# Kernel optimization log

Hardware: AMD Instinct MI355X
Metric: run time of the kernel (lower is better)

## Reference

```python
import jax, jax.numpy as jnp
import numpy as np

B, N, C, D = 64, 1024, 128, 64

def setup_inputs() -> dict:
    key = jax.random.key(0)
    ks = jax.random.split(key, 7)
    # kaiming_normal_ on weights (fan_in = C), default zero-ish biases kept as Linear default uniform; use small uniform
    std = float(np.sqrt(2.0 / C))
    bb = float(1.0 / np.sqrt(C))
    return {
        "x": jax.random.normal(ks[0], (B, N, C), jnp.float32),
        "Wq": jax.random.normal(ks[1], (C, D), jnp.float32) * std,
        "bq": jax.random.uniform(ks[2], (D,), jnp.float32, -bb, bb),
        "Wk": jax.random.normal(ks[3], (C, D), jnp.float32) * std,
        "bk": jax.random.uniform(ks[4], (D,), jnp.float32, -bb, bb),
        "Wv": jax.random.normal(ks[5], (C, D), jnp.float32) * std,
        "bv": jax.random.uniform(ks[6], (D,), jnp.float32, -bb, bb),
    }

def reference(x, Wq, bq, Wk, bk, Wv, bv):
    q = jax.nn.relu(jnp.einsum('bnc,cd->bnd', x, Wq) + bq)  # [B,N,D]
    k = jax.nn.relu(jnp.einsum('bnc,cd->bnd', x, Wk) + bk)
    v = jax.nn.relu(jnp.einsum('bnc,cd->bnd', x, Wv) + bv)
    scores = jnp.einsum('bnd,bmd->bnm', q, k) / jnp.sqrt(jnp.asarray(D, q.dtype))
    attn = jax.nn.softmax(scores, axis=-1)
    out = jnp.einsum('bnm,bmd->bnd', attn, v)
    return out + q
```

## Files before the change

kernel.cpp:

```cpp
#include <hip/hip_runtime.h>
#include <hip/hip_bf16.h>


#define Bsz 64
#define Nsz 1024
#define Csz 128
#define Dsz 64

typedef __attribute__((ext_vector_type(8))) short short8;
typedef __attribute__((ext_vector_type(4))) float f32x4;

__device__ __forceinline__ unsigned short f2bf(float f) {
    union { float f; unsigned u; } v; v.f = f;
    unsigned r = v.u + 0x7FFF + ((v.u >> 16) & 1);
    return (unsigned short)(r >> 16);
}
__device__ __forceinline__ float bf2f(unsigned short h) {
    union { unsigned u; float f; } v; v.u = ((unsigned)h) << 16;
    return v.f;
}
__device__ __forceinline__ unsigned pack_bf16rn(float lo, float hi) {
    unsigned ulo = __float_as_uint(lo) + 0x8000u;
    unsigned uhi = __float_as_uint(hi) + 0x8000u;
    return __builtin_amdgcn_perm(uhi, ulo, 0x07060302u);
}

#define SCq (0.125f * 1.44269504f)
#define INV_SC (1.0f / (0.125f * 1.44269504f))

__global__ __launch_bounds__(256) void wprep_kernel(
    const float* __restrict__ Wq, const float* __restrict__ Wk,
    const float* __restrict__ Wv, unsigned short* __restrict__ wfrag)
{
    int t = blockIdx.x * 256 + threadIdx.x;
    int lane = t & 63, ksi = (t >> 6) & 3, dt = t >> 8;
    int l16 = lane & 15, quad = lane >> 4;
    int d = dt * 16 + l16;
    int c0 = ksi * 32 + quad * 8;
    short8 h8, l8, k8, v8;
    #pragma unroll
    for (int j = 0; j < 8; j++) {
        float w = Wq[(c0 + j) * Dsz + d];
        unsigned short h = f2bf(w);
        h8[j] = (short)h;
        l8[j] = (short)f2bf(w - bf2f(h));
        k8[j] = (short)f2bf(Wk[(c0 + j) * Dsz + d]);
        v8[j] = (short)f2bf(Wv[(c0 + j) * Dsz + d]);
    }
    int idx = (dt * 4 + ksi) * 64 + lane;
    ((short8*)wfrag)[0 * 1024 + idx] = h8;
    ((short8*)wfrag)[1 * 1024 + idx] = l8;
    ((short8*)wfrag)[2 * 1024 + idx] = k8;
    ((short8*)wfrag)[3 * 1024 + idx] = v8;
}

__global__ __launch_bounds__(256) void qkv_kernel(
    const float* __restrict__ x, const unsigned short* __restrict__ wfrag,
    const float* __restrict__ bq, const float* __restrict__ bk,
    const float* __restrict__ bv,
    unsigned short* __restrict__ qs, unsigned short* __restrict__ ks2,
    unsigned short* __restrict__ vt2)
{
    __shared__ short xh[8192];
    __shared__ short xl[8192];
    const int t    = threadIdx.x;
    const int lane = t & 63;
    const int l16  = lane & 15, quad = lane >> 4;
    const int dt   = t >> 6;
    const int blk = blockIdx.x;
    const int r8  = blk & 7;
    const int m   = blk >> 3;
    const int bat = r8 + 8 * (m >> 4);
    const int til = m & 15;
    const long rowbase = ((long)bat * 16 + til) * 64;
    const int d = dt * 16 + l16;

    short8 wqh[4], wql[4], wkf[4], wvf[4];
    #pragma unroll
    for (int ksi = 0; ksi < 4; ksi++) {
        int idx = (dt * 4 + ksi) * 64 + lane;
        wqh[ksi] = ((const short8*)wfrag)[0 * 1024 + idx];
        wql[ksi] = ((const short8*)wfrag)[1 * 1024 + idx];
        wkf[ksi] = ((const short8*)wfrag)[2 * 1024 + idx];
        wvf[ksi] = ((const short8*)wfrag)[3 * 1024 + idx];
    }

    {
        const int row = t & 63;
        const float* xrow = x + (rowbase + row) * Csz;
        #pragma unroll
        for (int p = 0; p < 4; p++) {
            int cb = (t >> 6) + p * 4;
            float4 a = *(const float4*)(xrow + cb * 8);
            float4 bb = *(const float4*)(xrow + cb * 8 + 4);
            float f[8] = {a.x, a.y, a.z, a.w, bb.x, bb.y, bb.z, bb.w};
            short8 hi, lo;
            #pragma unroll
            for (int i = 0; i < 8; i++) {
                unsigned short h = f2bf(f[i]);
                hi[i] = (short)h;
                lo[i] = (short)f2bf(f[i] - bf2f(h));
            }
            int unit = ((row >> 4) * 4 + (cb >> 2)) * 64 + ((row & 15) | ((cb & 3) << 4));
            *(short8*)&xh[unit * 8] = hi;
            *(short8*)&xl[unit * 8] = lo;
        }
    }
    __syncthreads();

    f32x4 aq[4], ak[4], av[4];
    #pragma unroll
    for (int i = 0; i < 4; i++) {
        aq[i] = (f32x4){0.f, 0.f, 0.f, 0.f};
        ak[i] = (f32x4){0.f, 0.f, 0.f, 0.f};
        av[i] = (f32x4){0.f, 0.f, 0.f, 0.f};
    }
    #pragma unroll
    for (int ksi = 0; ksi < 4; ksi++) {
        #pragma unroll
        for (int rt = 0; rt < 4; rt++) {
            short8 ah = *(const short8*)&xh[((rt * 4 + ksi) * 64 + lane) * 8];
            short8 al = *(const short8*)&xl[((rt * 4 + ksi) * 64 + lane) * 8];
            aq[rt] = __builtin_amdgcn_mfma_f32_16x16x32_bf16(ah, wqh[ksi], aq[rt], 0, 0, 0);
            aq[rt] = __builtin_amdgcn_mfma_f32_16x16x32_bf16(al, wqh[ksi], aq[rt], 0, 0, 0);
            aq[rt] = __builtin_amdgcn_mfma_f32_16x16x32_bf16(ah, wql[ksi], aq[rt], 0, 0, 0);
            ak[rt] = __builtin_amdgcn_mfma_f32_16x16x32_bf16(ah, wkf[ksi], ak[rt], 0, 0, 0);
            av[rt] = __builtin_amdgcn_mfma_f32_16x16x32_bf16(ah, wvf[ksi], av[rt], 0, 0, 0);
        }
    }

    const float bqd = bq[d], bkd = bk[d], bvd = bv[d];
    const long b  = rowbase >> 10;
    const int  kt = (int)((rowbase >> 6) & 15);

    const int half  = dt >> 1;
    const int quadk = ((dt & 1) << 1) | (l16 >> 3);
    const int jk    = l16 & 7;
    unsigned short* kbase = ks2 + ((((long)(b * 16 + kt) * 4) * 2 + half) * 64) * 8;

    float vv[4][4];
    #pragma unroll
    for (int rt = 0; rt < 4; rt++) {
        #pragma unroll
        for (int r = 0; r < 4; r++) {
            long n = rowbase + rt * 16 + quad * 4 + r;
            float q = fmaxf(aq[rt][r] + bqd, 0.f);
            float k = fmaxf(ak[rt][r] + bkd, 0.f);
            vv[r][rt] = fmaxf(av[rt][r] + bvd, 0.f);
            qs[n * Dsz + d] = f2bf(q * SCq);
            kbase[((long)rt * 2 * 64 + quadk * 16 + quad * 4 + r) * 8 + jk] = f2bf(k);
        }
    }
    const int ck = quad >> 1;
    const int quadp = (quad & 1) * 2;
    long vidx = (((long)(b * 16 + kt) * 4 + dt) * 2 + ck) * 64 + quadp * 16 + l16;
    uint4 o0 = make_uint4(pack_bf16rn(vv[0][0], vv[0][1]), pack_bf16rn(vv[0][2], vv[0][3]),
                          pack_bf16rn(vv[1][0], vv[1][1]), pack_bf16rn(vv[1][2], vv[1][3]));
    uint4 o1 = make_uint4(pack_bf16rn(vv[2][0], vv[2][1]), pack_bf16rn(vv[2][2], vv[2][3]),
                          pack_bf16rn(vv[3][0], vv[3][1]), pack_bf16rn(vv[3][2], vv[3][3]));
    ((uint4*)vt2)[vidx]      = o0;
    ((uint4*)vt2)[vidx + 16] = o1;
}

__global__ __launch_bounds__(256) void attn_kernel(
    const unsigned short* __restrict__ qs,
    const unsigned short* __restrict__ ks2,
    const unsigned short* __restrict__ vt2,
    float* __restrict__ out)
{
    __shared__ short Pl[4][32][72];

    const int t    = threadIdx.x;
    const int wave = t >> 6;
    const int lane = t & 63;
    const int l16  = lane & 15;
    const int quad = lane >> 4;
    const int b    = blockIdx.x & 63;
    const int qh   = blockIdx.x >> 6;
    const int qbase = qh * 128 + wave * 32;

    const short8* ks8 = (const short8*)ks2 + (long)b * (16 * 4 * 2 * 64);
    const short8* vt8 = (const short8*)vt2 + (long)b * (16 * 4 * 2 * 64);

    short8 aq[2][2];
    #pragma unroll
    for (int s = 0; s < 2; s++) {
        const unsigned short* qp = qs + ((long)b * Nsz + qbase + s * 16 + l16) * Dsz + quad * 8;
        aq[s][0] = *(const short8*)(qp);
        aq[s][1] = *(const short8*)(qp + 32);
    }

    f32x4 O[2][4];
    float lsum[2][4];
    #pragma unroll
    for (int s = 0; s < 2; s++)
        #pragma unroll
        for (int i = 0; i < 4; i++) { O[s][i] = (f32x4){0.f,0.f,0.f,0.f}; lsum[s][i] = 0.f; }

    short8 kf[4][2];
    #pragma unroll
    for (int kb = 0; kb < 4; kb++) {
        kf[kb][0] = ks8[(kb * 2 + 0) * 64 + lane];
        kf[kb][1] = ks8[(kb * 2 + 1) * 64 + lane];
    }

    for (int kt = 0; kt < 16; kt++) {
        short8 bvf[2][4];
        #pragma unroll
        for (int cb = 0; cb < 4; cb++) {
            bvf[0][cb] = vt8[((long)kt * 8 + cb * 2 + 0) * 64 + lane];
            bvf[1][cb] = vt8[((long)kt * 8 + cb * 2 + 1) * 64 + lane];
        }

        f32x4 sc[2][4];
        #pragma unroll
        for (int s = 0; s < 2; s++) {
            #pragma unroll
            for (int kb = 0; kb < 4; kb++) {
                f32x4 z = (f32x4){0.f, 0.f, 0.f, 0.f};
                z = __builtin_amdgcn_mfma_f32_16x16x32_bf16(aq[s][0], kf[kb][0], z, 0, 0, 0);
                z = __builtin_amdgcn_mfma_f32_16x16x32_bf16(aq[s][1], kf[kb][1], z, 0, 0, 0);
                sc[s][kb] = z;
            }
        }

        short8 kf2[4][2];
        {
            int ktn = (kt + 1) & 15;
            #pragma unroll
            for (int kb = 0; kb < 4; kb++) {
                kf2[kb][0] = ks8[((long)ktn * 8 + kb * 2 + 0) * 64 + lane];
                kf2[kb][1] = ks8[((long)ktn * 8 + kb * 2 + 1) * 64 + lane];
            }
        }

        #pragma unroll
        for (int s = 0; s < 2; s++) {
            #pragma unroll
            for (int r = 0; r < 4; r++) {
                float p0 = __builtin_amdgcn_exp2f(sc[s][0][r]);
                float p1 = __builtin_amdgcn_exp2f(sc[s][1][r]);
                float p2 = __builtin_amdgcn_exp2f(sc[s][2][r]);
                float p3 = __builtin_amdgcn_exp2f(sc[s][3][r]);
                lsum[s][r] += (p0 + p1) + (p2 + p3);
                *(uint2*)&Pl[wave][s * 16 + quad * 4 + r][l16 * 4] =
                    make_uint2(pack_bf16rn(p0, p1), pack_bf16rn(p2, p3));
            }
        }

        #pragma unroll
        for (int ck = 0; ck < 2; ck++) {
            #pragma unroll
            for (int s = 0; s < 2; s++) {
                short8 ap = *(const short8*)&Pl[wave][s * 16 + l16][ck * 32 + quad * 8];
                #pragma unroll
                for (int cb = 0; cb < 4; cb++) {
                    O[s][cb] = __builtin_amdgcn_mfma_f32_16x16x32_bf16(ap, bvf[ck][cb], O[s][cb], 0, 0, 0);
                }
            }
        }

        #pragma unroll
        for (int kb = 0; kb < 4; kb++) { kf[kb][0] = kf2[kb][0]; kf[kb][1] = kf2[kb][1]; }
    }

    #pragma unroll
    for (int s = 0; s < 2; s++)
        #pragma unroll
        for (int r = 0; r < 4; r++)
            #pragma unroll
            for (int off = 1; off < 16; off <<= 1)
                lsum[s][r] += __shfl_xor(lsum[s][r], off);

    #pragma unroll
    for (int s = 0; s < 2; s++) {
        #pragma unroll
        for (int r = 0; r < 4; r++) {
            float rl = 1.0f / lsum[s][r];
            long nrow = (long)b * Nsz + qbase + s * 16 + quad * 4 + r;
            #pragma unroll
            for (int cb = 0; cb < 4; cb++) {
                int d = cb * 16 + l16;
                float qv = bf2f(qs[nrow * Dsz + d]) * INV_SC;
                out[nrow * Dsz + d] = O[s][cb][r] * rl + qv;
            }
        }
    }
}

extern "C" void kernel_launch(void* const* d_in, const int* in_sizes, int n_in,
                              void* d_out, int out_size, void* d_ws, size_t ws_size,
                              hipStream_t stream) {
    const float* x  = (const float*)d_in[0];
    const float* Wq = (const float*)d_in[1];
    const float* bq = (const float*)d_in[2];
    const float* Wk = (const float*)d_in[3];
    const float* bk = (const float*)d_in[4];
    const float* Wv = (const float*)d_in[5];
    const float* bv = (const float*)d_in[6];
    float* out = (float*)d_out;

    char* ws = (char*)d_ws;
    unsigned short* qsc   = (unsigned short*)ws;
    unsigned short* ks2   = (unsigned short*)(ws + 0x1000000);
    unsigned short* vt2   = (unsigned short*)(ws + 0x2000000);
    unsigned short* wfrag = (unsigned short*)(ws + 0x3000000);

    wprep_kernel<<<dim3(4), dim3(256), 0, stream>>>(Wq, Wk, Wv, wfrag);
    qkv_kernel<<<dim3(1024), dim3(256), 0, stream>>>(
        x, wfrag, bq, bk, bv, qsc, ks2, vt2);
    attn_kernel<<<dim3(512), dim3(256), 0, stream>>>(
        qsc, ks2, vt2, out);
}
```

Measured before the change: 122.8 us.

## Stage K/V tiles into LDS via async global_load_lds double buffering

The attention kernel now loads each K and V tile into a double-buffered LDS array with global_load_lds, split across waves: two waves fetch K and two fetch V. All four waves then read fragments from LDS instead of each wave loading them redundantly from global memory into registers. K is now stored row-major by the QKV kernel, so the fragment-swizzled K layout is dropped and the gather happens in the LDS staging addresses. This adds a __syncthreads per key tile and raises LDS use, with launch bounds now asking for 2 blocks per CU.

Result: no change. 123.6 us (+0.6%).

```diff
diff --git a/kernel.cpp b/kernel.cpp
--- a/kernel.cpp
+++ b/kernel.cpp
@@ -23,6 +23,12 @@
     unsigned ulo = __float_as_uint(lo) + 0x8000u;
     unsigned uhi = __float_as_uint(hi) + 0x8000u;
     return __builtin_amdgcn_perm(uhi, ulo, 0x07060302u);
+}
+__device__ __forceinline__ void gload_lds16(const void* gsrc, void* ldst) {
+    __builtin_amdgcn_global_load_lds(
+        (const __attribute__((address_space(1))) void*)gsrc,
+        (__attribute__((address_space(3))) void*)ldst,
+        16, 0, 0);
 }
 
 #define SCq (0.125f * 1.44269504f)
@@ -58,7 +64,7 @@
     const float* __restrict__ x, const unsigned short* __restrict__ wfrag,
     const float* __restrict__ bq, const float* __restrict__ bk,
     const float* __restrict__ bv,
-    unsigned short* __restrict__ qs, unsigned short* __restrict__ ks2,
+    unsigned short* __restrict__ qs, unsigned short* __restrict__ ksr,
     unsigned short* __restrict__ vt2)
 {
     __shared__ short xh[8192];
@@ -133,11 +139,6 @@
     const long b  = rowbase >> 10;
     const int  kt = (int)((rowbase >> 6) & 15);
 
-    const int half  = dt >> 1;
-    const int quadk = ((dt & 1) << 1) | (l16 >> 3);
-    const int jk    = l16 & 7;
-    unsigned short* kbase = ks2 + ((((long)(b * 16 + kt) * 4) * 2 + half) * 64) * 8;
-
     float vv[4][4];
     #pragma unroll
     for (int rt = 0; rt < 4; rt++) {
@@ -147,8 +148,8 @@
             float q = fmaxf(aq[rt][r] + bqd, 0.f);
             float k = fmaxf(ak[rt][r] + bkd, 0.f);
             vv[r][rt] = fmaxf(av[rt][r] + bvd, 0.f);
-            qs[n * Dsz + d] = f2bf(q * SCq);
-            kbase[((long)rt * 2 * 64 + quadk * 16 + quad * 4 + r) * 8 + jk] = f2bf(k);
+            qs[n * Dsz + d]  = f2bf(q * SCq);
+            ksr[n * Dsz + d] = f2bf(k);
         }
     }
     const int ck = quad >> 1;
@@ -162,12 +163,13 @@
     ((uint4*)vt2)[vidx + 16] = o1;
 }
 
-__global__ __launch_bounds__(256) void attn_kernel(
+__global__ __launch_bounds__(256, 2) void attn_kernel(
     const unsigned short* __restrict__ qs,
-    const unsigned short* __restrict__ ks2,
+    const unsigned short* __restrict__ ksr,
     const unsigned short* __restrict__ vt2,
     float* __restrict__ out)
 {
+    __shared__ short KV[2][16][512];
     __shared__ short Pl[4][32][72];
 
     const int t    = threadIdx.x;
@@ -179,8 +181,28 @@
     const int qh   = blockIdx.x >> 6;
     const int qbase = qh * 128 + wave * 32;
 
-    const short8* ks8 = (const short8*)ks2 + (long)b * (16 * 4 * 2 * 64);
+    const char*   kbR = (const char*)(ksr + (long)b * Nsz * Dsz);
     const short8* vt8 = (const short8*)vt2 + (long)b * (16 * 4 * 2 * 64);
+
+    auto stage = [&](int buf, int kt) {
+        if (wave < 2) {
+            #pragma unroll
+            for (int i = 0; i < 4; i++) {
+                int f = wave * 4 + i;
+                int kb = f >> 1, hf = f & 1;
+                const char* src = kbR + ((long)kt * 64 + kb * 16 + l16) * 128
+                                  + hf * 64 + quad * 16;
+                gload_lds16(src, &KV[buf][f][0]);
+            }
+        } else {
+            #pragma unroll
+            for (int i = 0; i < 4; i++) {
+                int f = (wave - 2) * 4 + i;
+                const short8* src = vt8 + ((long)kt * 8 + f) * 64 + lane;
+                gload_lds16(src, &KV[buf][8 + f][0]);
+            }
+        }
+    };
 
     short8 aq[2][2];
     #pragma unroll
@@ -197,19 +219,18 @@
         #pragma unroll
         for (int i = 0; i < 4; i++) { O[s][i] = (f32x4){0.f,0.f,0.f,0.f}; lsum[s][i] = 0.f; }
 
-    short8 kf[4][2];
-    #pragma unroll
-    for (int kb = 0; kb < 4; kb++) {
-        kf[kb][0] = ks8[(kb * 2 + 0) * 64 + lane];
-        kf[kb][1] = ks8[(kb * 2 + 1) * 64 + lane];
-    }
+    stage(0, 0);
+    __syncthreads();
 
     for (int kt = 0; kt < 16; kt++) {
-        short8 bvf[2][4];
-        #pragma unroll
-        for (int cb = 0; cb < 4; cb++) {
-            bvf[0][cb] = vt8[((long)kt * 8 + cb * 2 + 0) * 64 + lane];
-            bvf[1][cb] = vt8[((long)kt * 8 + cb * 2 + 1) * 64 + lane];
+        const int cur = kt & 1;
+        if (kt < 15) stage(cur ^ 1, kt + 1);
+
+        short8 kf[4][2];
+        #pragma unroll
+        for (int kb = 0; kb < 4; kb++) {
+            kf[kb][0] = *(const short8*)&KV[cur][kb * 2 + 0][lane * 8];
+            kf[kb][1] = *(const short8*)&KV[cur][kb * 2 + 1][lane * 8];
         }
 
         f32x4 sc[2][4];
@@ -224,14 +245,11 @@
             }
         }
 
-        short8 kf2[4][2];
-        {
-            int ktn = (kt + 1) & 15;
-            #pragma unroll
-            for (int kb = 0; kb < 4; kb++) {
-                kf2[kb][0] = ks8[((long)ktn * 8 + kb * 2 + 0) * 64 + lane];
-                kf2[kb][1] = ks8[((long)ktn * 8 + kb * 2 + 1) * 64 + lane];
-            }
+        short8 bvf[2][4];
+        #pragma unroll
+        for (int cb = 0; cb < 4; cb++) {
+            bvf[0][cb] = *(const short8*)&KV[cur][8 + cb * 2 + 0][lane * 8];
+            bvf[1][cb] = *(const short8*)&KV[cur][8 + cb * 2 + 1][lane * 8];
         }
 
         #pragma unroll
@@ -260,8 +278,7 @@
             }
         }
 
-        #pragma unroll
-        for (int kb = 0; kb < 4; kb++) { kf[kb][0] = kf2[kb][0]; kf[kb][1] = kf2[kb][1]; }
+        __syncthreads();
     }
 
     #pragma unroll
@@ -302,13 +319,13 @@
 
     char* ws = (char*)d_ws;
     unsigned short* qsc   = (unsigned short*)ws;
-    unsigned short* ks2   = (unsigned short*)(ws + 0x1000000);
+    unsigned short* ksr   = (unsigned short*)(ws + 0x1000000);
     unsigned short* vt2   = (unsigned short*)(ws + 0x2000000);
     unsigned short* wfrag = (unsigned short*)(ws + 0x3000000);
 
     wprep_kernel<<<dim3(4), dim3(256), 0, stream>>>(Wq, Wk, Wv, wfrag);
     qkv_kernel<<<dim3(1024), dim3(256), 0, stream>>>(
-        x, wfrag, bq, bk, bv, qsc, ks2, vt2);
+        x, wfrag, bq, bk, bv, qsc, ksr, vt2);
     attn_kernel<<<dim3(512), dim3(256), 0, stream>>>(
-        qsc, ks2, vt2, out);
-}
+        qsc, ksr, vt2, out);
+}
```
